# Kernel optimization log

Hardware: AMD Instinct MI355X
Metric: run time of the kernel (lower is better)

## Reference

```python
import jax, jax.numpy as jnp
import numpy as np

B, T, Fd, C, D = 16, 256, 128, 32, 32
K_RATIO = 0.5
EPS = 1e-5


def setup_inputs() -> dict:
    key = jax.random.key(0)
    ks = jax.random.split(key, 40)
    n = lambda i, shape, s=0.05: jax.random.normal(ks[i], shape, jnp.float32) * s
    inp = {"x": jax.random.normal(ks[0], (B, T, Fd, C), jnp.float32)}
    inp.update(c1w=n(1, (C, C)), c1b=n(2, (C,)), bng=1.0 + n(3, (C,)), bnb=n(4, (C,)),
               bnm=n(5, (C,)), bnv=jax.random.uniform(ks[6], (C,)) + 0.5,
               c2w=n(7, (1, C)), c2b=n(8, (1,)))
    def gat_params(i0, pre):
        return {pre + "apw": n(i0, (D, C)), pre + "apb": n(i0 + 1, (D,)),
                pre + "aw": n(i0 + 2, (D,)), pre + "pww": n(i0 + 3, (D, C)),
                pre + "pwb": n(i0 + 4, (D,)), pre + "pow": n(i0 + 5, (D, C)),
                pre + "pob": n(i0 + 6, (D,)), pre + "g": 1.0 + n(i0 + 7, (D,)),
                pre + "be": n(i0 + 8, (D,)), pre + "m": n(i0 + 9, (D,)),
                pre + "v": jax.random.uniform(ks[i0 + 10], (D,)) + 0.5}
    inp.update(gat_params(9, "fc_"))
    inp.update(gat_params(20, "tc_"))
    inp.update(pfw=n(31, (1, D)), pfb=n(32, (1,)), ptw=n(33, (1, D)), ptb=n(34, (1,)),
               w1=n(35, (D, D)), w2=n(36, (D, D)), fcw=n(37, (2, 2 * D)), fcb=n(38, (2,)))
    return inp


def _gat(h, apw, apb, aw, pww, pwb, poww, pob, g, be, mu, var):
    # h: (B, N, C). Dense pairwise multiplication -> (B, N, N, C)
    p = h[:, :, None, :] * h[:, None, :, :]
    e = jnp.tanh(jnp.einsum('bijc,dc->bijd', p, apw) + apb)      # (B,N,N,D)
    att = jax.nn.softmax(jnp.einsum('bijd,d->bij', e, aw), axis=2)  # softmax over dim=-2 (temp=1)
    out = jnp.einsum('bij,bjc->bic', att, h) @ pww.T + pwb + h @ poww.T + pob
    out = (out - mu) / jnp.sqrt(var + EPS) * g + be               # BatchNorm1d (eval)
    return jax.nn.selu(out)


def _pool(h, pw, pb, ratio):
    s = jax.nn.sigmoid(h @ pw.T + pb)                # (B,N,1)
    kn = max(int(h.shape[1] * ratio), 1)
    _, idx = jax.lax.top_k(s[..., 0], kn)            # (B,kn), descending scores
    return jnp.take_along_axis(h * s, idx[..., None], axis=1)


def reference(x, c1w, c1b, bng, bnb, bnm, bnv, c2w, c2b,
              fc_apw, fc_apb, fc_aw, fc_pww, fc_pwb, fc_pow, fc_pob, fc_g, fc_be, fc_m, fc_v,
              tc_apw, tc_apb, tc_aw, tc_pww, tc_pwb, tc_pow, tc_pob, tc_g, tc_be, tc_m, tc_v,
              pfw, pfb, ptw, ptb, w1, w2, fcw, fcb):
    # conv1 (1x1), SELU, BatchNorm2d (eval), conv2 (1x1 -> 1 channel)
    xp = jnp.einsum('oc,btfc->botf', c1w, x) + c1b[None, :, None, None]
    xp = jax.nn.selu(xp)
    xp = (xp - bnm[None, :, None, None]) / jnp.sqrt(bnv + EPS)[None, :, None, None] \
         * bng[None, :, None, None] + bnb[None, :, None, None]
    m = jnp.einsum('c,bctf->btf', c2w[0], xp) + c2b[0]           # (B,T,F)
    M0 = jax.nn.softmax(m, axis=1)
    FCatt = jnp.einsum('btf,btfc->bfc', M0, x)                   # sum over T
    TCatt = jnp.einsum('btf,btfc->btc', M0, x)                   # sum over F
    FC_gat = _gat(FCatt, fc_apw, fc_apb, fc_aw, fc_pww, fc_pwb, fc_pow, fc_pob, fc_g, fc_be, fc_m, fc_v)
    TC_gat = _gat(TCatt, tc_apw, tc_apb, tc_aw, tc_pww, tc_pwb, tc_pow, tc_pob, tc_g, tc_be, tc_m, tc_v)
    xF = _pool(FC_gat, pfw, pfb, K_RATIO)                        # (B, F/2, D)
    xT = _pool(TC_gat, ptw, ptb, K_RATIO)                        # (B, T/2, D)
    M1 = jax.nn.softmax((xF @ w1.T) @ xT.transpose(0, 2, 1), axis=-1)
    M2 = jax.nn.softmax((xT @ w2.T) @ xF.transpose(0, 2, 1), axis=-1)
    xF_fused = xF + M1 @ xT
    xT_fused = xT + M2 @ xF
    node = jnp.concatenate([xF_fused.max(axis=1), xT_fused.max(axis=1)], axis=-1)
    return node @ fcw.T + fcb
```

## Files before the change

kernel.cpp:

```cpp
#include <hip/hip_runtime.h>
#include <hip/hip_bf16.h>

#define Bn 16
#define Tn 256
#define Fn 128
#define Cn 32
#define Dn 32
#define EPSf 1e-5f
#define SELU_L 1.0507009873554805f
#define SELU_A 1.6732632423543772f

typedef unsigned short u16;
typedef unsigned int u32;
typedef __attribute__((ext_vector_type(8))) short bf16x8;
typedef __attribute__((ext_vector_type(4))) float f32x4;

struct Ptrs { const void* p[39]; };

#define P_C1W 0
#define P_C1B 1024
#define P_MW  1056
#define P_MK  1088
#define P_FC  1089
#define P_TCG (1089+3264)
#define G_APW 0
#define G_APB 1024
#define G_AW  1056
#define G_PWW 1088
#define G_PWB 2112
#define G_POW 2144
#define G_POB 3168
#define G_GS  3200
#define G_GB  3232
#define GAT_SZ 3264
#define P_PFW (P_TCG+GAT_SZ)
#define P_PFB (P_PFW+32)
#define P_PTW (P_PFB+1)
#define P_PTB (P_PTW+32)
#define P_W1  (P_PTB+1)
#define P_W2  (P_W1+1024)
#define P_FCW (P_W2+1024)
#define P_FCB (P_FCW+128)
#define P_FLAG 10000

#define WS_M     10240
#define WS_FCATT (WS_M+524288)
#define WS_TCATT (WS_FCATT+65536)
#define WS_FCGAT (WS_TCATT+131072)
#define WS_TCGAT (WS_FCGAT+65536)
#define WS_XF    (WS_TCGAT+131072)
#define WS_XT    (WS_XF+32768)
#define WS_XFF   (WS_XT+65536)
#define WS_XTF   (WS_XFF+32768)

__device__ __forceinline__ float bf2f(u16 u) {
    union { u32 i; float f; } v; v.i = ((u32)u) << 16; return v.f;
}
__device__ __forceinline__ u16 f2bf(float f) {
    union { float f; u32 u; } v; v.f = f;
    u32 r = (v.u + 0x7fffu + ((v.u >> 16) & 1u)) >> 16;
    return (u16)r;
}
__device__ __forceinline__ u32 cvt_pk_bf16(float lo, float hi) {
    u32 r;
    asm("v_cvt_pk_bf16_f32 %0, %1, %2" : "=v"(r) : "v"(lo), "v"(hi));
    return r;
}
__device__ __forceinline__ void up2(u32 u, float* o) {
    union { u32 i; float f; } a, b;
    a.i = u << 16; b.i = u & 0xffff0000u;
    o[0] = a.f; o[1] = b.f;
}
__device__ __forceinline__ float tanh_fast(float x) {
    float e = __expf(2.f * x);
    return 1.f - 2.f / (e + 1.f);
}
__device__ __forceinline__ float ldp(const void* p, int i, int isb) {
    return isb ? bf2f(((const u16*)p)[i]) : ((const float*)p)[i];
}

__global__ __launch_bounds__(256) void k0_setup(Ptrs in, float* __restrict__ P) {
    __shared__ int sflag;
    int tid = threadIdx.x;
    int blk = blockIdx.x;
    if (tid < 64) {
        const u16* xu = (const u16*)in.p[0];
        int bad = 0;
        #pragma unroll
        for (int q = 0; q < 4; q++) {
            float f = bf2f(xu[tid * 4 + q]);
            float a = fabsf(f);
            if (!(a < 64.f) && !(a == 0.f)) bad++;
        }
        #pragma unroll
        for (int off = 32; off >= 1; off >>= 1) bad += __shfl_xor(bad, off, 64);
        if (tid == 0) sflag = (bad <= 8) ? 1 : 0;
    }
    __syncthreads();
    const int isb = sflag;

    if (blk == 0) {
        if (tid == 0) P[P_FLAG] = (float)isb;
        for (int i = tid; i < 1024; i += 256) P[P_C1W + i] = ldp(in.p[1], i, isb);
        if (tid < 32) {
            float A = ldp(in.p[3], tid, isb) * rsqrtf(ldp(in.p[6], tid, isb) + EPSf);
            float w = ldp(in.p[7], tid, isb);
            P[P_C1B + tid] = ldp(in.p[2], tid, isb);
            P[P_MW + tid] = w * A * SELU_L;
            float Bc = ldp(in.p[4], tid, isb) - ldp(in.p[5], tid, isb) * A;
            float term = w * Bc;
            #pragma unroll
            for (int off = 16; off >= 1; off >>= 1) term += __shfl_xor(term, off, 64);
            if (tid == 0) P[P_MK] = term + ldp(in.p[8], 0, isb);
        }
        if (tid >= 64 && tid < 96) {
            int t = tid - 64;
            P[P_PFW + t] = ldp(in.p[31], t, isb);
            P[P_PTW + t] = ldp(in.p[33], t, isb);
        }
        if (tid == 96) { P[P_PFB] = ldp(in.p[32], 0, isb); P[P_PTB] = ldp(in.p[34], 0, isb); }
        if (tid == 97) P[P_FCB]     = ldp(in.p[38], 0, isb);
        if (tid == 98) P[P_FCB + 1] = ldp(in.p[38], 1, isb);
        if (tid >= 128) P[P_FCW + (tid - 128)] = ldp(in.p[37], tid - 128, isb);
    } else if (blk <= 2) {
        int g = blk - 1;
        int ib = g ? 20 : 9;
        float* G = P + (g ? P_TCG : P_FC);
        for (int i = tid; i < 1024; i += 256) {
            G[G_APW + i] = ldp(in.p[ib + 0], i, isb);
            G[G_PWW + i] = ldp(in.p[ib + 3], i, isb);
            G[G_POW + i] = ldp(in.p[ib + 5], i, isb);
        }
        if (tid < 32) {
            G[G_APB + tid] = ldp(in.p[ib + 1], tid, isb);
            G[G_AW  + tid] = ldp(in.p[ib + 2], tid, isb);
            G[G_PWB + tid] = ldp(in.p[ib + 4], tid, isb);
            G[G_POB + tid] = ldp(in.p[ib + 6], tid, isb);
            float gs = ldp(in.p[ib + 7], tid, isb) * rsqrtf(ldp(in.p[ib + 10], tid, isb) + EPSf);
            G[G_GS + tid] = gs;
            G[G_GB + tid] = ldp(in.p[ib + 8], tid, isb) - ldp(in.p[ib + 9], tid, isb) * gs;
        }
    } else {
        for (int i = tid; i < 1024; i += 256) {
            P[P_W1 + i] = ldp(in.p[35], i, isb);
            P[P_W2 + i] = ldp(in.p[36], i, isb);
        }
    }
}

__global__ __launch_bounds__(256) void k1_conv_m(const void* __restrict__ xin,
                                                 const float* __restrict__ P,
                                                 float* __restrict__ M) {
    const int isb = __builtin_amdgcn_readfirstlane((int)P[P_FLAG]);
    int tid = threadIdx.x;
    if (isb) {
        int w = tid >> 6, lane = tid & 63;
        int n = lane & 15, g = lane >> 4, kc = g * 8;
        union { u32 u[4]; bf16x8 v; } B0, B1;
        #pragma unroll
        for (int e = 0; e < 4; e++) {
            B0.u[e] = cvt_pk_bf16(P[P_C1W + n * 32 + kc + 2 * e],
                                  P[P_C1W + n * 32 + kc + 2 * e + 1]);
            B1.u[e] = cvt_pk_bf16(P[P_C1W + (n + 16) * 32 + kc + 2 * e],
                                  P[P_C1W + (n + 16) * 32 + kc + 2 * e + 1]);
        }
        float cb0v[4], cb1v[4], mw0v[4], mw1v[4];
        #pragma unroll
        for (int r = 0; r < 4; r++) {
            cb0v[r] = P[P_C1B + g * 4 + r];
            cb1v[r] = P[P_C1B + 16 + g * 4 + r];
            mw0v[r] = P[P_MW + g * 4 + r];
            mw1v[r] = P[P_MW + 16 + g * 4 + r];
        }
        float mk = P[P_MK];
        int rowblk = blockIdx.x * 256 + w * 64;
        const u16* xp = (const u16*)xin + (size_t)rowblk * 32;
        bf16x8 a[4];
        #pragma unroll
        for (int s = 0; s < 4; s++)
            a[s] = *(const bf16x8*)(xp + ((size_t)s * 16 + n) * 32 + kc);
        #pragma unroll
        for (int s = 0; s < 4; s++) {
            f32x4 c0 = {0.f, 0.f, 0.f, 0.f}, c1 = {0.f, 0.f, 0.f, 0.f};
            c0 = __builtin_amdgcn_mfma_f32_16x16x32_bf16(B0.v, a[s], c0, 0, 0, 0);
            c1 = __builtin_amdgcn_mfma_f32_16x16x32_bf16(B1.v, a[s], c1, 0, 0, 0);
            float part = 0.f;
            #pragma unroll
            for (int r = 0; r < 4; r++) {
                float z0 = c0[r] + cb0v[r], z1 = c1[r] + cb1v[r];
                float s0 = (z0 > 0.f) ? z0 : SELU_A * (__expf(z0) - 1.f);
                float s1 = (z1 > 0.f) ? z1 : SELU_A * (__expf(z1) - 1.f);
                part = fmaf(mw0v[r], s0, part);
                part = fmaf(mw1v[r], s1, part);
            }
            part += __shfl_xor(part, 16, 64);
            part += __shfl_xor(part, 32, 64);
            if (lane < 16) M[(size_t)rowblk + s * 16 + n] = part + mk;
        }
    } else {
        int idx = blockIdx.x * 256 + tid;
        float xv[32];
        const float4* xf4 = reinterpret_cast<const float4*>((const float*)xin + (size_t)idx * 32);
        #pragma unroll
        for (int q = 0; q < 8; q++) {
            float4 v = xf4[q];
            xv[q * 4 + 0] = v.x; xv[q * 4 + 1] = v.y;
            xv[q * 4 + 2] = v.z; xv[q * 4 + 3] = v.w;
        }
        float acc = P[P_MK];
        #pragma unroll
        for (int o = 0; o < 32; o++) {
            float z = P[P_C1B + o];
            #pragma unroll
            for (int c = 0; c < 32; c++) z = fmaf(P[P_C1W + o * 32 + c], xv[c], z);
            float br = (z > 0.f) ? z : SELU_A * (__expf(z) - 1.f);
            acc = fmaf(P[P_MW + o], br, acc);
        }
        M[idx] = acc;
    }
}

__global__ __launch_bounds__(256) void k2_softmax(float* __restrict__ M,
                                                  float* __restrict__ FCzero) {
    __shared__ float r[256];
    int b = blockIdx.x >> 3, fg = blockIdx.x & 7;
    int tid = threadIdx.x;
    int fl = tid & 15, ts = tid >> 4;
    float* col = M + (size_t)b * (Tn * Fn) + fg * 16 + fl;
    float v[16];
    float mx = -1e30f;
    #pragma unroll
    for (int k = 0; k < 16; k++) { v[k] = col[(ts * 16 + k) * Fn]; mx = fmaxf(mx, v[k]); }
    r[tid] = mx; __syncthreads();
    for (int s = 128; s >= 16; s >>= 1) { if (tid < s) r[tid] = fmaxf(r[tid], r[tid + s]); __syncthreads(); }
    mx = r[fl];
    __syncthreads();
    float sm = 0.f;
    #pragma unroll
    for (int k = 0; k < 16; k++) { v[k] = __expf(v[k] - mx); sm += v[k]; }
    r[tid] = sm; __syncthreads();
    for (int s = 128; s >= 16; s >>= 1) { if (tid < s) r[tid] += r[tid + s]; __syncthreads(); }
    float inv = 1.f / r[fl];
    #pragma unroll
    for (int k = 0; k < 16; k++) col[(ts * 16 + k) * Fn] = v[k] * inv;
    int gid = blockIdx.x * 256 + tid;
    for (int i = gid; i < Bn * Fn * Cn; i += 128 * 256) FCzero[i] = 0.f;
}

__global__ __launch_bounds__(256) void k3n(const void* __restrict__ xin,
                                           const float* __restrict__ M,
                                           const float* __restrict__ Pflag,
                                           float* __restrict__ FCatt,
                                           float* __restrict__ TCatt) {
    __shared__ float part[4][8][32];
    int bi = blockIdx.x;
    int b = bi >> 5, tg = bi & 31;
    int tid = threadIdx.x;
    int w = tid >> 6, lane = tid & 63;
    const int isb = __builtin_amdgcn_readfirstlane((int)Pflag[P_FLAG]);
    float fa0[8], fa1[8];
    #pragma unroll
    for (int k = 0; k < 8; k++) { fa0[k] = 0.f; fa1[k] = 0.f; }
    int fbase = tid >> 4;
    for (int tt = 0; tt < 8; tt++) {
        int t = tg * 8 + tt;
        const float* Mrow = M + (size_t)b * (Tn * Fn) + (size_t)t * Fn;
        size_t rowoff = ((size_t)b * Tn + t) * (Fn * Cn);
        float ts0 = 0.f, ts1 = 0.f;
        #pragma unroll
        for (int k = 0; k < 8; k++) {
            float x0, x1;
            if (isb) {
                u32 u = *(const u32*)((const u16*)xin + rowoff + tid * 2 + 512 * k);
                float tmp[2]; up2(u, tmp); x0 = tmp[0]; x1 = tmp[1];
            } else {
                float2 v2 = *(const float2*)((const float*)xin + rowoff + tid * 2 + 512 * k);
                x0 = v2.x; x1 = v2.y;
            }
            float m = Mrow[fbase + 16 * k];
            x0 *= m; x1 *= m;
            fa0[k] += x0; fa1[k] += x1;
            ts0 += x0; ts1 += x1;
        }
        ts0 += __shfl_xor(ts0, 16, 64); ts0 += __shfl_xor(ts0, 32, 64);
        ts1 += __shfl_xor(ts1, 16, 64); ts1 += __shfl_xor(ts1, 32, 64);
        if (lane < 16) {
            part[w][tt][lane * 2]     = ts0;
            part[w][tt][lane * 2 + 1] = ts1;
        }
    }
    __syncthreads();
    {
        int tt = tid >> 5, c = tid & 31;
        float s = part[0][tt][c] + part[1][tt][c] + part[2][tt][c] + part[3][tt][c];
        TCatt[((size_t)b * Tn + tg * 8 + tt) * Cn + c] = s;
    }
    #pragma unroll
    for (int k = 0; k < 8; k++) {
        atomicAdd(&FCatt[(size_t)b * 4096 + tid * 2 + 512 * k],     fa0[k]);
        atomicAdd(&FCatt[(size_t)b * 4096 + tid * 2 + 512 * k + 1], fa1[k]);
    }
}

__global__ __launch_bounds__(256) void k4a_scores(const float* __restrict__ P,
                                                  const float* __restrict__ FCatt,
                                                  const float* __restrict__ TCatt,
                                                  u16* __restrict__ SFC,
                                                  u16* __restrict__ STC) {
    int bi = blockIdx.x;
    int tid = threadIdx.x;
    int w = tid >> 6, lane = tid & 63;
    int n = lane & 15, g = lane >> 4, kc = g * 8;
    int N, b, i, jt0; const float* h; u16* S; const float* G;
    if (bi < 512) {
        N = 128; b = bi >> 5; i = (bi & 31) * 4 + w; jt0 = 0;
        h = FCatt + (size_t)b * 4096; S = SFC + (size_t)b * 16384; G = P + P_FC;
    } else {
        int unit = (bi - 512) * 4 + w;
        N = 256; b = unit >> 9;
        int rem = unit & 511;
        i = rem >> 1; jt0 = (rem & 1) * 8;
        h = TCatt + (size_t)b * 8192; S = STC + (size_t)b * 65536; G = P + P_TCG;
    }

    union { u32 u[4]; bf16x8 v; } B0, B1;
    #pragma unroll
    for (int e = 0; e < 4; e++) {
        B0.u[e] = cvt_pk_bf16(G[G_APW + n * 32 + kc + 2 * e],
                              G[G_APW + n * 32 + kc + 2 * e + 1]);
        B1.u[e] = cvt_pk_bf16(G[G_APW + (n + 16) * 32 + kc + 2 * e],
                              G[G_APW + (n + 16) * 32 + kc + 2 * e + 1]);
    }
    float awv0[4], awv1[4], abv0[4], abv1[4];
    #pragma unroll
    for (int r = 0; r < 4; r++) {
        awv0[r] = G[G_AW + g * 4 + r];
        awv1[r] = G[G_AW + 16 + g * 4 + r];
        abv0[r] = G[G_APB + g * 4 + r];
        abv1[r] = G[G_APB + 16 + g * 4 + r];
    }

    float hi[8];
    {
        const float4* hip = (const float4*)(h + (size_t)i * 32 + kc);
        float4 v0 = hip[0], v1 = hip[1];
        hi[0] = v0.x; hi[1] = v0.y; hi[2] = v0.z; hi[3] = v0.w;
        hi[4] = v1.x; hi[5] = v1.y; hi[6] = v1.z; hi[7] = v1.w;
    }

    #pragma unroll 2
    for (int q = 0; q < 8; q++) {
        int jt = jt0 + q;
        const float4* hjp = (const float4*)(h + ((size_t)jt * 16 + n) * 32 + kc);
        float4 v0 = hjp[0], v1 = hjp[1];
        union { u32 u[4]; bf16x8 v; } A;
        A.u[0] = cvt_pk_bf16(hi[0] * v0.x, hi[1] * v0.y);
        A.u[1] = cvt_pk_bf16(hi[2] * v0.z, hi[3] * v0.w);
        A.u[2] = cvt_pk_bf16(hi[4] * v1.x, hi[5] * v1.y);
        A.u[3] = cvt_pk_bf16(hi[6] * v1.z, hi[7] * v1.w);
        f32x4 c0 = {0.f, 0.f, 0.f, 0.f}, c1 = {0.f, 0.f, 0.f, 0.f};
        c0 = __builtin_amdgcn_mfma_f32_16x16x32_bf16(B0.v, A.v, c0, 0, 0, 0);
        c1 = __builtin_amdgcn_mfma_f32_16x16x32_bf16(B1.v, A.v, c1, 0, 0, 0);
        float part = 0.f;
        #pragma unroll
        for (int r = 0; r < 4; r++) {
            part = fmaf(awv0[r], tanh_fast(c0[r] + abv0[r]), part);
            part = fmaf(awv1[r], tanh_fast(c1[r] + abv1[r]), part);
        }
        part += __shfl_xor(part, 16, 64);
        part += __shfl_xor(part, 32, 64);
        if (lane < 16) S[(size_t)i * N + jt * 16 + n] = f2bf(part);
    }
}

__global__ __launch_bounds__(256) void k4b_soft(const float* __restrict__ P,
                                                const float* __restrict__ FCatt,
                                                const float* __restrict__ TCatt,
                                                const u16* __restrict__ SFC,
                                                const u16* __restrict__ STC,
                                                float* __restrict__ FCgat,
                                                float* __restrict__ TCgat) {
    __shared__ float hs[256 * 32];
    __shared__ float scb[4][256];
    int bi = blockIdx.x;
    int N, b, rowbase; const float* h; float* out; const float* G; const u16* S;
    if (bi < 128) {
        N = 128; b = bi >> 3; rowbase = (bi & 7) * 16;
        h = FCatt + (size_t)b * 4096; out = FCgat + (size_t)b * 4096; G = P + P_FC;
        S = SFC + (size_t)b * 16384;
    } else {
        int t = bi - 128;
        N = 256; b = t >> 4; rowbase = (t & 15) * 16;
        h = TCatt + (size_t)b * 8192; out = TCgat + (size_t)b * 8192; G = P + P_TCG;
        S = STC + (size_t)b * 65536;
    }
    int tid = threadIdx.x;
    int w = tid >> 6, lane = tid & 63;
    const float4* h4 = reinterpret_cast<const float4*>(h);
    float4* hs4 = reinterpret_cast<float4*>(hs);
    for (int el = tid; el < N * 8; el += 256) hs4[el] = h4[el];
    __syncthreads();

    int c = lane & 31;
    int nq = N >> 6;
    for (int r = 0; r < 4; r++) {
        int row = rowbase + w + 4 * r;
        const u16* Srow = S + (size_t)row * N;
        float v[4];
        float mx = -1e30f;
        for (int q = 0; q < nq; q++) { v[q] = bf2f(Srow[lane + 64 * q]); mx = fmaxf(mx, v[q]); }
        #pragma unroll
        for (int off = 32; off >= 1; off >>= 1) mx = fmaxf(mx, __shfl_xor(mx, off, 64));
        float sum = 0.f;
        for (int q = 0; q < nq; q++) {
            float e = __expf(v[q] - mx);
            scb[w][lane + 64 * q] = e;
            sum += e;
        }
        #pragma unroll
        for (int off = 32; off >= 1; off >>= 1) sum += __shfl_xor(sum, off, 64);
        float inv = 1.f / sum;
        asm volatile("s_waitcnt lgkmcnt(0)" ::: "memory");
        int half = lane >> 5;
        float acc = 0.f;
        for (int j = half; j < N; j += 2) acc = fmaf(scb[w][j], hs[j * 32 + c], acc);
        acc += __shfl_xor(acc, 32, 64);
        acc *= inv;
        int d = c;
        float z = G[G_PWB + d] + G[G_POB + d];
        #pragma unroll
        for (int c2 = 0; c2 < 32; c2++)
            z = fmaf(G[G_PWW + d * 32 + c2], __shfl(acc, c2, 64),
                fmaf(G[G_POW + d * 32 + c2], hs[row * 32 + c2], z));
        z = z * G[G_GS + d] + G[G_GB + d];
        z = SELU_L * ((z > 0.f) ? z : SELU_A * (__expf(z) - 1.f));
        if (lane < 32) out[(size_t)row * 32 + d] = z;
    }
}

__global__ __launch_bounds__(256) void k5_pool(const float* __restrict__ P,
                                               const float* __restrict__ FCgat,
                                               const float* __restrict__ TCgat,
                                               float* __restrict__ XF,
                                               float* __restrict__ XT) {
    __shared__ float s[256];
    int bi = blockIdx.x;
    int N, kn, b, pboff; const float* g; float* xp; const float* pw;
    if (bi < 16) { b = bi; N = 128; kn = 64;
        g = FCgat + (size_t)b * 4096; xp = XF + (size_t)b * 2048; pw = P + P_PFW; pboff = P_PFB; }
    else { b = bi - 16; N = 256; kn = 128;
        g = TCgat + (size_t)b * 8192; xp = XT + (size_t)b * 4096; pw = P + P_PTW; pboff = P_PTB; }
    int tid = threadIdx.x;
    float sv = 0.f;
    if (tid < N) {
        float z = P[pboff];
        #pragma unroll
        for (int d = 0; d < 32; d++) z = fmaf(pw[d], g[(size_t)tid * 32 + d], z);
        sv = 1.f / (1.f + __expf(-z));
        s[tid] = sv;
    }
    __syncthreads();
    if (tid < N) {
        int rank = 0;
        for (int l = 0; l < N; l++) {
            float sl = s[l];
            rank += (sl > sv) || (sl == sv && l < tid);
        }
        if (rank < kn) {
            #pragma unroll
            for (int d = 0; d < 32; d++) xp[(size_t)rank * 32 + d] = g[(size_t)tid * 32 + d] * sv;
        }
    }
}

__global__ __launch_bounds__(256) void k6_fuse(const float* __restrict__ P,
                                               const float* __restrict__ XF,
                                               const float* __restrict__ XT,
                                               float* __restrict__ XFF,
                                               float* __restrict__ XTF) {
    int wid = blockIdx.x * 4 + (threadIdx.x >> 6);
    int lane = threadIdx.x & 63;
    if (wid < 1024) {
        int b = wid >> 6, i = wid & 63;
        const float* xf  = XF + ((size_t)b * 64 + i) * 32;
        const float* xtb = XT + (size_t)b * 4096;
        const float* w1 = P + P_W1;
        int d = lane & 31;
        float y = 0.f;
        #pragma unroll
        for (int c = 0; c < 32; c++) y = fmaf(w1[d * 32 + c], xf[c], y);
        float xtr0[32], xtr1[32];
        #pragma unroll
        for (int c = 0; c < 32; c++) {
            xtr0[c] = xtb[(size_t)lane * 32 + c];
            xtr1[c] = xtb[(size_t)(lane + 64) * 32 + c];
        }
        float s0 = 0.f, s1 = 0.f;
        #pragma unroll
        for (int c = 0; c < 32; c++) {
            float yc = __shfl(y, c, 64);
            s0 = fmaf(yc, xtr0[c], s0);
            s1 = fmaf(yc, xtr1[c], s1);
        }
        float mx = fmaxf(s0, s1);
        #pragma unroll
        for (int off = 1; off < 64; off <<= 1) mx = fmaxf(mx, __shfl_xor(mx, off, 64));
        float e0 = __expf(s0 - mx), e1 = __expf(s1 - mx);
        float sm = e0 + e1;
        #pragma unroll
        for (int off = 1; off < 64; off <<= 1) sm += __shfl_xor(sm, off, 64);
        float inv = 1.f / sm;
        float a0 = e0 * inv, a1 = e1 * inv;
        float v[32];
        #pragma unroll
        for (int c = 0; c < 32; c++) v[c] = a0 * xtr0[c] + a1 * xtr1[c];
        #pragma unroll
        for (int off = 1; off < 64; off <<= 1) {
            #pragma unroll
            for (int c = 0; c < 32; c++) v[c] += __shfl_xor(v[c], off, 64);
        }
        if (lane == 0) {
            float* o = XFF + ((size_t)b * 64 + i) * 32;
            #pragma unroll
            for (int c = 0; c < 32; c++) o[c] = xf[c] + v[c];
        }
    } else {
        int r = wid - 1024;
        int b = r >> 7, i = r & 127;
        const float* xt  = XT + ((size_t)b * 128 + i) * 32;
        const float* xfb = XF + (size_t)b * 2048;
        const float* w2 = P + P_W2;
        int d = lane & 31;
        float y = 0.f;
        #pragma unroll
        for (int c = 0; c < 32; c++) y = fmaf(w2[d * 32 + c], xt[c], y);
        float xfr[32];
        #pragma unroll
        for (int c = 0; c < 32; c++) xfr[c] = xfb[(size_t)lane * 32 + c];
        float sc0 = 0.f;
        #pragma unroll
        for (int c = 0; c < 32; c++) sc0 = fmaf(__shfl(y, c, 64), xfr[c], sc0);
        float mx = sc0;
        #pragma unroll
        for (int off = 1; off < 64; off <<= 1) mx = fmaxf(mx, __shfl_xor(mx, off, 64));
        float e = __expf(sc0 - mx);
        float sm = e;
        #pragma unroll
        for (int off = 1; off < 64; off <<= 1) sm += __shfl_xor(sm, off, 64);
        float a = e / sm;
        float v[32];
        #pragma unroll
        for (int c = 0; c < 32; c++) v[c] = a * xfr[c];
        #pragma unroll
        for (int off = 1; off < 64; off <<= 1) {
            #pragma unroll
            for (int c = 0; c < 32; c++) v[c] += __shfl_xor(v[c], off, 64);
        }
        if (lane == 0) {
            float* o = XTF + ((size_t)b * 128 + i) * 32;
            #pragma unroll
            for (int c = 0; c < 32; c++) o[c] = xt[c] + v[c];
        }
    }
}

__global__ __launch_bounds__(64) void k7_out(const float* __restrict__ P,
                                             const float* __restrict__ XFF,
                                             const float* __restrict__ XTF,
                                             void* __restrict__ outp) {
    __shared__ float node[64];
    int b = blockIdx.x, tid = threadIdx.x;
    if (tid < 32) {
        float m = -1e30f;
        for (int r = 0; r < 64; r++) m = fmaxf(m, XFF[((size_t)b * 64 + r) * 32 + tid]);
        node[tid] = m;
    } else {
        int c = tid - 32;
        float m = -1e30f;
        for (int r = 0; r < 128; r++) m = fmaxf(m, XTF[((size_t)b * 128 + r) * 32 + c]);
        node[tid] = m;
    }
    __syncthreads();
    if (tid < 2) {
        float z = P[P_FCB + tid];
        #pragma unroll
        for (int k = 0; k < 64; k++) z = fmaf(P[P_FCW + tid * 64 + k], node[k], z);
        int isb = (int)P[P_FLAG];
        if (isb) ((u16*)outp)[b * 2 + tid] = f2bf(z);
        else     ((float*)outp)[b * 2 + tid] = z;
    }
}

extern "C" void kernel_launch(void* const* d_in, const int* in_sizes, int n_in,
                              void* d_out, int out_size, void* d_ws, size_t ws_size,
                              hipStream_t stream) {
    (void)in_sizes; (void)n_in; (void)out_size; (void)ws_size;
    float* W = (float*)d_ws;
    Ptrs ptrs;
    for (int i = 0; i < 39; i++) ptrs.p[i] = d_in[i];
    const void* x = d_in[0];
    float* P = W;
    u16* STC = (u16*)(W + WS_M);
    u16* SFC = (u16*)(W + WS_XF);

    k0_setup<<<4, 256, 0, stream>>>(ptrs, P);
    k1_conv_m<<<2048, 256, 0, stream>>>(x, P, W + WS_M);
    k2_softmax<<<128, 256, 0, stream>>>(W + WS_M, W + WS_FCATT);
    k3n<<<512, 256, 0, stream>>>(x, W + WS_M, P, W + WS_FCATT, W + WS_TCATT);
    k4a_scores<<<2560, 256, 0, stream>>>(P, W + WS_FCATT, W + WS_TCATT, SFC, STC);
    k4b_soft<<<384, 256, 0, stream>>>(P, W + WS_FCATT, W + WS_TCATT, SFC, STC,
                                      W + WS_FCGAT, W + WS_TCGAT);
    k5_pool<<<32, 256, 0, stream>>>(P, W + WS_FCGAT, W + WS_TCGAT, W + WS_XF, W + WS_XT);
    k6_fuse<<<768, 256, 0, stream>>>(P, W + WS_XF, W + WS_XT, W + WS_XFF, W + WS_XTF);
    k7_out<<<16, 64, 0, stream>>>(P, W + WS_XFF, W + WS_XTF, d_out);
}
```

Before: 336.1 us.

## Vectorize softmax and attention-pooling loads, fuse pool/fuse/output kernels into one

The T-softmax kernel now uses float4 loads with wave-shuffle reductions instead of a shared-memory tree, and the FC/TC attention-pooling kernel reads contiguous 8-element chunks per lane instead of strided pairs. The three tail kernels (top-k pooling, cross-attention fusion, max+linear output) are merged into one block per batch that keeps intermediates in LDS. This removes two launches and the global round-trips for the tail, but runs the fusion stage on only 16 blocks, so it has far less parallelism than the old 768-block launch.

```diff
diff --git a/kernel.cpp b/kernel.cpp
--- a/kernel.cpp
+++ b/kernel.cpp
@@ -222,27 +222,65 @@
 
 __global__ __launch_bounds__(256) void k2_softmax(float* __restrict__ M,
                                                   float* __restrict__ FCzero) {
-    __shared__ float r[256];
+    __shared__ float wred[4][16];
     int b = blockIdx.x >> 3, fg = blockIdx.x & 7;
     int tid = threadIdx.x;
-    int fl = tid & 15, ts = tid >> 4;
-    float* col = M + (size_t)b * (Tn * Fn) + fg * 16 + fl;
-    float v[16];
-    float mx = -1e30f;
-    #pragma unroll
-    for (int k = 0; k < 16; k++) { v[k] = col[(ts * 16 + k) * Fn]; mx = fmaxf(mx, v[k]); }
-    r[tid] = mx; __syncthreads();
-    for (int s = 128; s >= 16; s >>= 1) { if (tid < s) r[tid] = fmaxf(r[tid], r[tid + s]); __syncthreads(); }
-    mx = r[fl];
-    __syncthreads();
-    float sm = 0.f;
-    #pragma unroll
-    for (int k = 0; k < 16; k++) { v[k] = __expf(v[k] - mx); sm += v[k]; }
-    r[tid] = sm; __syncthreads();
-    for (int s = 128; s >= 16; s >>= 1) { if (tid < s) r[tid] += r[tid + s]; __syncthreads(); }
-    float inv = 1.f / r[fl];
-    #pragma unroll
-    for (int k = 0; k < 16; k++) col[(ts * 16 + k) * Fn] = v[k] * inv;
+    int w = tid >> 6, lane = tid & 63;
+    int fq = tid & 3, tt = tid >> 2;
+    float* colb = M + (size_t)b * (Tn * Fn) + fg * 16 + fq * 4;
+    float4 v[4];
+    float mx[4] = {-1e30f, -1e30f, -1e30f, -1e30f};
+    #pragma unroll
+    for (int p = 0; p < 4; p++) {
+        v[p] = *(float4*)(colb + (size_t)(tt + p * 64) * Fn);
+        mx[0] = fmaxf(mx[0], v[p].x); mx[1] = fmaxf(mx[1], v[p].y);
+        mx[2] = fmaxf(mx[2], v[p].z); mx[3] = fmaxf(mx[3], v[p].w);
+    }
+    #pragma unroll
+    for (int off = 4; off <= 32; off <<= 1) {
+        #pragma unroll
+        for (int c = 0; c < 4; c++) mx[c] = fmaxf(mx[c], __shfl_xor(mx[c], off, 64));
+    }
+    if (lane < 4) {
+        #pragma unroll
+        for (int c = 0; c < 4; c++) wred[w][lane * 4 + c] = mx[c];
+    }
+    __syncthreads();
+    #pragma unroll
+    for (int c = 0; c < 4; c++)
+        mx[c] = fmaxf(fmaxf(wred[0][fq * 4 + c], wred[1][fq * 4 + c]),
+                      fmaxf(wred[2][fq * 4 + c], wred[3][fq * 4 + c]));
+    float4 e[4];
+    float sm[4] = {0.f, 0.f, 0.f, 0.f};
+    #pragma unroll
+    for (int p = 0; p < 4; p++) {
+        e[p].x = __expf(v[p].x - mx[0]); sm[0] += e[p].x;
+        e[p].y = __expf(v[p].y - mx[1]); sm[1] += e[p].y;
+        e[p].z = __expf(v[p].z - mx[2]); sm[2] += e[p].z;
+        e[p].w = __expf(v[p].w - mx[3]); sm[3] += e[p].w;
+    }
+    #pragma unroll
+    for (int off = 4; off <= 32; off <<= 1) {
+        #pragma unroll
+        for (int c = 0; c < 4; c++) sm[c] += __shfl_xor(sm[c], off, 64);
+    }
+    __syncthreads();
+    if (lane < 4) {
+        #pragma unroll
+        for (int c = 0; c < 4; c++) wred[w][lane * 4 + c] = sm[c];
+    }
+    __syncthreads();
+    float inv[4];
+    #pragma unroll
+    for (int c = 0; c < 4; c++)
+        inv[c] = 1.f / (wred[0][fq * 4 + c] + wred[1][fq * 4 + c] +
+                        wred[2][fq * 4 + c] + wred[3][fq * 4 + c]);
+    #pragma unroll
+    for (int p = 0; p < 4; p++) {
+        float4 o4 = make_float4(e[p].x * inv[0], e[p].y * inv[1],
+                                e[p].z * inv[2], e[p].w * inv[3]);
+        *(float4*)(colb + (size_t)(tt + p * 64) * Fn) = o4;
+    }
     int gid = blockIdx.x * 256 + tid;
     for (int i = gid; i < Bn * Fn * Cn; i += 128 * 256) FCzero[i] = 0.f;
 }
@@ -257,36 +295,50 @@
     int b = bi >> 5, tg = bi & 31;
     int tid = threadIdx.x;
     int w = tid >> 6, lane = tid & 63;
+    int cc = (tid & 3) * 8, f0 = tid >> 2;
     const int isb = __builtin_amdgcn_readfirstlane((int)Pflag[P_FLAG]);
     float fa0[8], fa1[8];
     #pragma unroll
-    for (int k = 0; k < 8; k++) { fa0[k] = 0.f; fa1[k] = 0.f; }
-    int fbase = tid >> 4;
+    for (int e = 0; e < 8; e++) { fa0[e] = 0.f; fa1[e] = 0.f; }
     for (int tt = 0; tt < 8; tt++) {
         int t = tg * 8 + tt;
         const float* Mrow = M + (size_t)b * (Tn * Fn) + (size_t)t * Fn;
+        float m0 = Mrow[f0], m1 = Mrow[f0 + 64];
         size_t rowoff = ((size_t)b * Tn + t) * (Fn * Cn);
-        float ts0 = 0.f, ts1 = 0.f;
-        #pragma unroll
-        for (int k = 0; k < 8; k++) {
-            float x0, x1;
-            if (isb) {
-                u32 u = *(const u32*)((const u16*)xin + rowoff + tid * 2 + 512 * k);
-                float tmp[2]; up2(u, tmp); x0 = tmp[0]; x1 = tmp[1];
-            } else {
-                float2 v2 = *(const float2*)((const float*)xin + rowoff + tid * 2 + 512 * k);
-                x0 = v2.x; x1 = v2.y;
-            }
-            float m = Mrow[fbase + 16 * k];
-            x0 *= m; x1 *= m;
-            fa0[k] += x0; fa1[k] += x1;
-            ts0 += x0; ts1 += x1;
-        }
-        ts0 += __shfl_xor(ts0, 16, 64); ts0 += __shfl_xor(ts0, 32, 64);
-        ts1 += __shfl_xor(ts1, 16, 64); ts1 += __shfl_xor(ts1, 32, 64);
-        if (lane < 16) {
-            part[w][tt][lane * 2]     = ts0;
-            part[w][tt][lane * 2 + 1] = ts1;
+        float xv0[8], xv1[8];
+        if (isb) {
+            const u16* xr = (const u16*)xin + rowoff + f0 * 32 + cc;
+            union { u32 u[4]; bf16x8 v; } q0, q1;
+            q0.v = *(const bf16x8*)xr;
+            q1.v = *(const bf16x8*)(xr + 64 * 32);
+            up2(q0.u[0], xv0 + 0); up2(q0.u[1], xv0 + 2);
+            up2(q0.u[2], xv0 + 4); up2(q0.u[3], xv0 + 6);
+            up2(q1.u[0], xv1 + 0); up2(q1.u[1], xv1 + 2);
+            up2(q1.u[2], xv1 + 4); up2(q1.u[3], xv1 + 6);
+        } else {
+            const float* xr = (const float*)xin + rowoff + f0 * 32 + cc;
+            float4 a0 = *(const float4*)xr, a1 = *(const float4*)(xr + 4);
+            float4 b0 = *(const float4*)(xr + 64 * 32), b1 = *(const float4*)(xr + 64 * 32 + 4);
+            xv0[0] = a0.x; xv0[1] = a0.y; xv0[2] = a0.z; xv0[3] = a0.w;
+            xv0[4] = a1.x; xv0[5] = a1.y; xv0[6] = a1.z; xv0[7] = a1.w;
+            xv1[0] = b0.x; xv1[1] = b0.y; xv1[2] = b0.z; xv1[3] = b0.w;
+            xv1[4] = b1.x; xv1[5] = b1.y; xv1[6] = b1.z; xv1[7] = b1.w;
+        }
+        float tp[8];
+        #pragma unroll
+        for (int e = 0; e < 8; e++) {
+            float p0 = xv0[e] * m0, p1 = xv1[e] * m1;
+            fa0[e] += p0; fa1[e] += p1;
+            tp[e] = p0 + p1;
+        }
+        #pragma unroll
+        for (int off = 4; off <= 32; off <<= 1) {
+            #pragma unroll
+            for (int e = 0; e < 8; e++) tp[e] += __shfl_xor(tp[e], off, 64);
+        }
+        if (lane < 4) {
+            #pragma unroll
+            for (int e = 0; e < 8; e++) part[w][tt][lane * 8 + e] = tp[e];
         }
     }
     __syncthreads();
@@ -296,9 +348,9 @@
         TCatt[((size_t)b * Tn + tg * 8 + tt) * Cn + c] = s;
     }
     #pragma unroll
-    for (int k = 0; k < 8; k++) {
-        atomicAdd(&FCatt[(size_t)b * 4096 + tid * 2 + 512 * k],     fa0[k]);
-        atomicAdd(&FCatt[(size_t)b * 4096 + tid * 2 + 512 * k + 1], fa1[k]);
+    for (int e = 0; e < 8; e++) {
+        atomicAdd(&FCatt[(size_t)b * 4096 + f0 * 32 + cc + e],        fa0[e]);
+        atomicAdd(&FCatt[(size_t)b * 4096 + (f0 + 64) * 32 + cc + e], fa1[e]);
     }
 }
 
@@ -438,146 +490,144 @@
     }
 }
 
-__global__ __launch_bounds__(256) void k5_pool(const float* __restrict__ P,
-                                               const float* __restrict__ FCgat,
-                                               const float* __restrict__ TCgat,
-                                               float* __restrict__ XF,
-                                               float* __restrict__ XT) {
-    __shared__ float s[256];
-    int bi = blockIdx.x;
-    int N, kn, b, pboff; const float* g; float* xp; const float* pw;
-    if (bi < 16) { b = bi; N = 128; kn = 64;
-        g = FCgat + (size_t)b * 4096; xp = XF + (size_t)b * 2048; pw = P + P_PFW; pboff = P_PFB; }
-    else { b = bi - 16; N = 256; kn = 128;
-        g = TCgat + (size_t)b * 8192; xp = XT + (size_t)b * 4096; pw = P + P_PTW; pboff = P_PTB; }
+__global__ __launch_bounds__(256) void k567(const float* __restrict__ P,
+                                            const float* __restrict__ FCgat,
+                                            const float* __restrict__ TCgat,
+                                            void* __restrict__ outp) {
+    __shared__ float s_fc[128], s_tc[256];
+    __shared__ float XFL[64][33], XTL[128][33];
+    __shared__ float XFFL[64][33], XTFL[128][33];
+    __shared__ float node[64];
+    int b = blockIdx.x;
     int tid = threadIdx.x;
-    float sv = 0.f;
-    if (tid < N) {
-        float z = P[pboff];
-        #pragma unroll
-        for (int d = 0; d < 32; d++) z = fmaf(pw[d], g[(size_t)tid * 32 + d], z);
-        sv = 1.f / (1.f + __expf(-z));
-        s[tid] = sv;
-    }
-    __syncthreads();
-    if (tid < N) {
+    int w = tid >> 6, lane = tid & 63;
+    const float* gfc = FCgat + (size_t)b * 4096;
+    const float* gtc = TCgat + (size_t)b * 8192;
+
+    {
+        float z = P[P_PTB];
+        const float* row = gtc + (size_t)tid * 32;
+        #pragma unroll
+        for (int d = 0; d < 32; d++) z = fmaf(P[P_PTW + d], row[d], z);
+        s_tc[tid] = 1.f / (1.f + __expf(-z));
+        if (tid < 128) {
+            float z2 = P[P_PFB];
+            const float* row2 = gfc + (size_t)tid * 32;
+            #pragma unroll
+            for (int d = 0; d < 32; d++) z2 = fmaf(P[P_PFW + d], row2[d], z2);
+            s_fc[tid] = 1.f / (1.f + __expf(-z2));
+        }
+    }
+    __syncthreads();
+    {
+        float sv = s_tc[tid];
         int rank = 0;
-        for (int l = 0; l < N; l++) {
-            float sl = s[l];
+        for (int l = 0; l < 256; l++) {
+            float sl = s_tc[l];
             rank += (sl > sv) || (sl == sv && l < tid);
         }
-        if (rank < kn) {
-            #pragma unroll
-            for (int d = 0; d < 32; d++) xp[(size_t)rank * 32 + d] = g[(size_t)tid * 32 + d] * sv;
-        }
-    }
-}
-
-__global__ __launch_bounds__(256) void k6_fuse(const float* __restrict__ P,
-                                               const float* __restrict__ XF,
-                                               const float* __restrict__ XT,
-                                               float* __restrict__ XFF,
-                                               float* __restrict__ XTF) {
-    int wid = blockIdx.x * 4 + (threadIdx.x >> 6);
-    int lane = threadIdx.x & 63;
-    if (wid < 1024) {
-        int b = wid >> 6, i = wid & 63;
-        const float* xf  = XF + ((size_t)b * 64 + i) * 32;
-        const float* xtb = XT + (size_t)b * 4096;
-        const float* w1 = P + P_W1;
-        int d = lane & 31;
-        float y = 0.f;
-        #pragma unroll
-        for (int c = 0; c < 32; c++) y = fmaf(w1[d * 32 + c], xf[c], y);
-        float xtr0[32], xtr1[32];
-        #pragma unroll
-        for (int c = 0; c < 32; c++) {
-            xtr0[c] = xtb[(size_t)lane * 32 + c];
-            xtr1[c] = xtb[(size_t)(lane + 64) * 32 + c];
-        }
-        float s0 = 0.f, s1 = 0.f;
-        #pragma unroll
-        for (int c = 0; c < 32; c++) {
-            float yc = __shfl(y, c, 64);
-            s0 = fmaf(yc, xtr0[c], s0);
-            s1 = fmaf(yc, xtr1[c], s1);
-        }
-        float mx = fmaxf(s0, s1);
-        #pragma unroll
-        for (int off = 1; off < 64; off <<= 1) mx = fmaxf(mx, __shfl_xor(mx, off, 64));
-        float e0 = __expf(s0 - mx), e1 = __expf(s1 - mx);
-        float sm = e0 + e1;
-        #pragma unroll
-        for (int off = 1; off < 64; off <<= 1) sm += __shfl_xor(sm, off, 64);
-        float inv = 1.f / sm;
-        float a0 = e0 * inv, a1 = e1 * inv;
-        float v[32];
-        #pragma unroll
-        for (int c = 0; c < 32; c++) v[c] = a0 * xtr0[c] + a1 * xtr1[c];
-        #pragma unroll
-        for (int off = 1; off < 64; off <<= 1) {
-            #pragma unroll
-            for (int c = 0; c < 32; c++) v[c] += __shfl_xor(v[c], off, 64);
-        }
-        if (lane == 0) {
-            float* o = XFF + ((size_t)b * 64 + i) * 32;
-            #pragma unroll
-            for (int c = 0; c < 32; c++) o[c] = xf[c] + v[c];
-        }
-    } else {
-        int r = wid - 1024;
-        int b = r >> 7, i = r & 127;
-        const float* xt  = XT + ((size_t)b * 128 + i) * 32;
-        const float* xfb = XF + (size_t)b * 2048;
-        const float* w2 = P + P_W2;
-        int d = lane & 31;
-        float y = 0.f;
-        #pragma unroll
-        for (int c = 0; c < 32; c++) y = fmaf(w2[d * 32 + c], xt[c], y);
-        float xfr[32];
-        #pragma unroll
-        for (int c = 0; c < 32; c++) xfr[c] = xfb[(size_t)lane * 32 + c];
-        float sc0 = 0.f;
-        #pragma unroll
-        for (int c = 0; c < 32; c++) sc0 = fmaf(__shfl(y, c, 64), xfr[c], sc0);
-        float mx = sc0;
-        #pragma unroll
-        for (int off = 1; off < 64; off <<= 1) mx = fmaxf(mx, __shfl_xor(mx, off, 64));
-        float e = __expf(sc0 - mx);
-        float sm = e;
-        #pragma unroll
-        for (int off = 1; off < 64; off <<= 1) sm += __shfl_xor(sm, off, 64);
-        float a = e / sm;
-        float v[32];
-        #pragma unroll
-        for (int c = 0; c < 32; c++) v[c] = a * xfr[c];
-        #pragma unroll
-        for (int off = 1; off < 64; off <<= 1) {
-            #pragma unroll
-            for (int c = 0; c < 32; c++) v[c] += __shfl_xor(v[c], off, 64);
-        }
-        if (lane == 0) {
-            float* o = XTF + ((size_t)b * 128 + i) * 32;
-            #pragma unroll
-            for (int c = 0; c < 32; c++) o[c] = xt[c] + v[c];
-        }
-    }
-}
-
-__global__ __launch_bounds__(64) void k7_out(const float* __restrict__ P,
-                                             const float* __restrict__ XFF,
-                                             const float* __restrict__ XTF,
-                                             void* __restrict__ outp) {
-    __shared__ float node[64];
-    int b = blockIdx.x, tid = threadIdx.x;
+        if (rank < 128) {
+            #pragma unroll
+            for (int d = 0; d < 32; d++) XTL[rank][d] = gtc[(size_t)tid * 32 + d] * sv;
+        }
+        if (tid < 128) {
+            float sf = s_fc[tid];
+            int rk = 0;
+            for (int l = 0; l < 128; l++) {
+                float sl = s_fc[l];
+                rk += (sl > sf) || (sl == sf && l < tid);
+            }
+            if (rk < 64) {
+                #pragma unroll
+                for (int d = 0; d < 32; d++) XFL[rk][d] = gfc[(size_t)tid * 32 + d] * sf;
+            }
+        }
+    }
+    __syncthreads();
+    const float* w1 = P + P_W1;
+    const float* w2 = P + P_W2;
+    for (int q = w; q < 192; q += 4) {
+        if (q < 64) {
+            int i = q, d = lane & 31;
+            float y = 0.f;
+            #pragma unroll
+            for (int c = 0; c < 32; c++) y = fmaf(w1[d * 32 + c], XFL[i][c], y);
+            float xtr0[32], xtr1[32];
+            #pragma unroll
+            for (int c = 0; c < 32; c++) {
+                xtr0[c] = XTL[lane][c];
+                xtr1[c] = XTL[lane + 64][c];
+            }
+            float s0 = 0.f, s1 = 0.f;
+            #pragma unroll
+            for (int c = 0; c < 32; c++) {
+                float yc = __shfl(y, c, 64);
+                s0 = fmaf(yc, xtr0[c], s0);
+                s1 = fmaf(yc, xtr1[c], s1);
+            }
+            float mx = fmaxf(s0, s1);
+            #pragma unroll
+            for (int off = 1; off < 64; off <<= 1) mx = fmaxf(mx, __shfl_xor(mx, off, 64));
+            float e0 = __expf(s0 - mx), e1 = __expf(s1 - mx);
+            float sm = e0 + e1;
+            #pragma unroll
+            for (int off = 1; off < 64; off <<= 1) sm += __shfl_xor(sm, off, 64);
+            float inv = 1.f / sm;
+            float a0 = e0 * inv, a1 = e1 * inv;
+            float v[32];
+            #pragma unroll
+            for (int c = 0; c < 32; c++) v[c] = a0 * xtr0[c] + a1 * xtr1[c];
+            #pragma unroll
+            for (int off = 1; off < 64; off <<= 1) {
+                #pragma unroll
+                for (int c = 0; c < 32; c++) v[c] += __shfl_xor(v[c], off, 64);
+            }
+            if (lane == 0) {
+                #pragma unroll
+                for (int c = 0; c < 32; c++) XFFL[i][c] = XFL[i][c] + v[c];
+            }
+        } else {
+            int i = q - 64, d = lane & 31;
+            float y = 0.f;
+            #pragma unroll
+            for (int c = 0; c < 32; c++) y = fmaf(w2[d * 32 + c], XTL[i][c], y);
+            float xfr[32];
+            #pragma unroll
+            for (int c = 0; c < 32; c++) xfr[c] = XFL[lane & 63][c];
+            float sc0 = 0.f;
+            #pragma unroll
+            for (int c = 0; c < 32; c++) sc0 = fmaf(__shfl(y, c, 64), xfr[c], sc0);
+            float mx = sc0;
+            #pragma unroll
+            for (int off = 1; off < 64; off <<= 1) mx = fmaxf(mx, __shfl_xor(mx, off, 64));
+            float e = __expf(sc0 - mx);
+            float sm = e;
+            #pragma unroll
+            for (int off = 1; off < 64; off <<= 1) sm += __shfl_xor(sm, off, 64);
+            float a = e / sm;
+            float v[32];
+            #pragma unroll
+            for (int c = 0; c < 32; c++) v[c] = a * xfr[c];
+            #pragma unroll
+            for (int off = 1; off < 64; off <<= 1) {
+                #pragma unroll
+                for (int c = 0; c < 32; c++) v[c] += __shfl_xor(v[c], off, 64);
+            }
+            if (lane == 0) {
+                #pragma unroll
+                for (int c = 0; c < 32; c++) XTFL[i][c] = XTL[i][c] + v[c];
+            }
+        }
+    }
+    __syncthreads();
     if (tid < 32) {
         float m = -1e30f;
-        for (int r = 0; r < 64; r++) m = fmaxf(m, XFF[((size_t)b * 64 + r) * 32 + tid]);
+        for (int r = 0; r < 64; r++) m = fmaxf(m, XFFL[r][tid]);
         node[tid] = m;
-    } else {
+    } else if (tid < 64) {
         int c = tid - 32;
         float m = -1e30f;
-        for (int r = 0; r < 128; r++) m = fmaxf(m, XTF[((size_t)b * 128 + r) * 32 + c]);
+        for (int r = 0; r < 128; r++) m = fmaxf(m, XTFL[r][c]);
         node[tid] = m;
     }
     __syncthreads();
@@ -610,7 +660,5 @@
     k4a_scores<<<2560, 256, 0, stream>>>(P, W + WS_FCATT, W + WS_TCATT, SFC, STC);
     k4b_soft<<<384, 256, 0, stream>>>(P, W + WS_FCATT, W + WS_TCATT, SFC, STC,
                                       W + WS_FCGAT, W + WS_TCGAT);
-    k5_pool<<<32, 256, 0, stream>>>(P, W + WS_FCGAT, W + WS_TCGAT, W + WS_XF, W + WS_XT);
-    k6_fuse<<<768, 256, 0, stream>>>(P, W + WS_XF, W + WS_XT, W + WS_XFF, W + WS_XTF);
-    k7_out<<<16, 64, 0, stream>>>(P, W + WS_XFF, W + WS_XTF, d_out);
-}
+    k567<<<16, 256, 0, stream>>>(P, W + WS_FCGAT, W + WS_TCGAT, d_out);
+}
```

Result: slower. 485.5 us (+44.5%).
